# Optimization experiments

Hardware: AMD Instinct MI355X
Metric: run time of the kernel (lower is better)

Reference implementation:

```python
import jax, jax.numpy as jnp
import numpy as np

TEMPERATURE = 0.05
BETA = 1.0
LAMBDA_THRESHOLD = 0.7


def setup_inputs() -> dict:
    key = jax.random.key(0)
    k1, k2 = jax.random.split(key)
    B, D = 8192, 256
    features = jax.random.normal(k1, (B, D), dtype=jnp.float32)
    labels = jax.random.randint(k2, (B,), 0, 100, dtype=jnp.int64)
    return {"features": features, "labels": labels}


def reference(features, labels):
    B = features.shape[0]
    eps = 1e-12
    # L2 normalize rows
    f = features / jnp.maximum(jnp.linalg.norm(features, axis=1, keepdims=True), eps)
    sim = jnp.matmul(f, f.T) / TEMPERATURE                      # [B, B]
    sim_max = jnp.max(sim, axis=1, keepdims=True)               # [B, 1]
    sim_stable = sim - sim_max

    same = (labels[:, None] == labels[None, :])
    eye = jnp.eye(B, dtype=bool)
    pos_mask = same & ~eye                                       # [B, B] bool

    # Denominator: logsumexp over all non-self entries per row
    exp_sim = jnp.exp(sim_stable) * (~eye)
    log_denom = jnp.log(jnp.sum(exp_sim, axis=1, keepdims=True) + eps) + sim_max  # [B,1]

    # SCL term: mean over positive pairs of (log_denom[i] - sim[i,j])
    pos_f = pos_mask.astype(sim.dtype)
    n_pos = jnp.sum(pos_f)
    scl_sum = jnp.sum(pos_f * (log_denom - sim))
    scl_loss = jnp.where(n_pos > 0, scl_sum / jnp.maximum(n_pos, 1.0), 0.0)

    # Relaxation term: per row, logsumexp over high-sim positive logits + baseline
    high = (sim * TEMPERATURE > LAMBDA_THRESHOLD) & pos_mask     # [B, B] bool
    neg_inf = jnp.asarray(-jnp.inf, sim.dtype)
    masked_logits = jnp.where(high, sim_stable, neg_inf)          # [B, B]
    baseline = (1.0 / TEMPERATURE) - sim_max                      # [B, 1]
    all_logits = jnp.concatenate([masked_logits, baseline], axis=1)  # [B, B+1]
    row_lse = jax.nn.logsumexp(all_logits, axis=1)                # [B]
    row_has = jnp.any(high, axis=1)
    n_high = jnp.sum(high.astype(sim.dtype))
    relax_sum = jnp.sum(jnp.where(row_has, row_lse, 0.0))
    relaxation_loss = jnp.where(n_high > 0, relax_sum / jnp.maximum(n_high, 1.0), 0.0)

    total = scl_loss + BETA * relaxation_loss
    return jnp.clip(total, 0.0, 10.0)
```

## Files before the change

### kernel.cpp

```cpp
#include <hip/hip_runtime.h>
#include <hip/hip_bf16.h>
#include <math.h>

#define B_N 8192
#define D_K 256
#define TILE 128
#define NT 512
#define NBLK 64
#define NPAIR 2080
#define NCLS 100
#define KEXP 28.8539008177792681f
#define KCH 32
#define NCHUNK 8

typedef __attribute__((ext_vector_type(8))) short short8;
typedef __attribute__((ext_vector_type(4))) float f32x4;

template <bool V> struct BoolC { static constexpr bool value = V; };

__device__ __forceinline__ unsigned short f2bf(float x) {
    unsigned int u = __float_as_uint(x);
    unsigned int r = (u + 0x7FFFu + ((u >> 16) & 1u)) >> 16;
    return (unsigned short)r;
}

__device__ __forceinline__ void gload_lds16(const short* g, short* l) {
    __builtin_amdgcn_global_load_lds(
        (const __attribute__((address_space(1))) void*)g,
        (__attribute__((address_space(3))) void*)l, 16, 0, 0);
}

__device__ __forceinline__ float row_sum16(float v) {
    v += __int_as_float(__builtin_amdgcn_update_dpp(0, __float_as_int(v), 0xB1, 0xF, 0xF, true));
    v += __int_as_float(__builtin_amdgcn_update_dpp(0, __float_as_int(v), 0x4E, 0xF, 0xF, true));
    v += __int_as_float(__builtin_amdgcn_update_dpp(0, __float_as_int(v), 0x141, 0xF, 0xF, true));
    v += __int_as_float(__builtin_amdgcn_update_dpp(0, __float_as_int(v), 0x140, 0xF, 0xF, true));
    return v;
}

__global__ void prep_kernel(const float* __restrict__ feat, unsigned short* __restrict__ fnorm,
                            const int* __restrict__ labels, int* __restrict__ cnt,
                            float* __restrict__ gscal, double* __restrict__ accum,
                            unsigned int* __restrict__ done) {
    if (blockIdx.x == 0) {
        __shared__ int h[NCLS];
        int t = threadIdx.x;
        if (t < NCLS) h[t] = 0;
        if (t == 0) {
            gscal[0] = 0.f; gscal[1] = 0.f;
            accum[0] = 0.0; accum[1] = 0.0; accum[2] = 0.0;
            *done = 0u;
        }
        __syncthreads();
        for (int r = t; r < B_N; r += 256) atomicAdd(&h[labels[r]], 1);
        __syncthreads();
        if (t < NCLS) cnt[t] = h[t];
    }
    int wave = threadIdx.x >> 6, lane = threadIdx.x & 63;
    int row = blockIdx.x * 4 + wave;
    float4 v = *(const float4*)(feat + (size_t)row * D_K + lane * 4);
    float ss = v.x * v.x + v.y * v.y + v.z * v.z + v.w * v.w;
    #pragma unroll
    for (int off = 1; off < 64; off <<= 1) ss += __shfl_xor(ss, off);
    float inv = 1.0f / fmaxf(sqrtf(ss), 1e-12f);
    ushort4 o;
    o.x = f2bf(v.x * inv); o.y = f2bf(v.y * inv);
    o.z = f2bf(v.z * inv); o.w = f2bf(v.w * inv);
    *(ushort4*)(fnorm + (size_t)row * D_K + lane * 4) = o;
}

#define WAITV(N) asm volatile("s_waitcnt vmcnt(" #N ")" ::: "memory")
#define BARX() __builtin_amdgcn_s_barrier()

__global__ __launch_bounds__(NT, 4) void main_kernel(
        const unsigned short* __restrict__ fnorm, const int* __restrict__ labels,
        float2* __restrict__ G, float* __restrict__ gscal) {
    int bid = blockIdx.x;
    int b = (int)((sqrtf(8.0f * bid + 1.0f) - 1.0f) * 0.5f);
    while ((b + 1) * (b + 2) / 2 <= bid) ++b;
    while (b * (b + 1) / 2 > bid) --b;
    int a = bid - b * (b + 1) / 2;
    const int row0 = a * TILE, col0 = b * TILE;
    const bool diag = (a == b);

    __shared__ short As[4][TILE * KCH];
    __shared__ short Bs[4][TILE * KCH];
    __shared__ int Ls[2 * TILE];
    __shared__ float2 Rbuf[4 * TILE];
    __shared__ float2 Cbuf[2 * TILE];
    __shared__ int ghs[8];
    __shared__ float gps[8];

    const int tid = threadIdx.x;
    const int lane = tid & 63, wave = tid >> 6;
    const int wm = wave >> 2, wn = wave & 3;
    const int l15 = lane & 15, lhi = lane >> 4;
    const short* fn = (const short*)fnorm;

    const int rs = tid >> 2, cs = (tid & 3) ^ ((tid >> 3) & 3);
    const int uds = (tid & ~63) * 8;
    const int abase = (row0 + rs) * D_K + cs * 8;
    const int bbase = (col0 + rs) * D_K + cs * 8;

    if (tid < 128) Ls[tid] = labels[row0 + tid];
    else if (tid < 256) Ls[tid] = labels[col0 + tid - 128];
    if (lane == 0) ghs[wave] = 0;

    const int ch8 = (lhi ^ ((l15 >> 1) & 3)) * 8;
    int aoff[4], boff[2];
    #pragma unroll
    for (int mi = 0; mi < 4; mi++) aoff[mi] = (wm * 64 + mi * 16 + l15) * KCH + ch8;
    #pragma unroll
    for (int ni = 0; ni < 2; ni++) boff[ni] = (wn * 32 + ni * 16 + l15) * KCH + ch8;

    f32x4 acc[4][2];
    #pragma unroll
    for (int i = 0; i < 4; i++)
        #pragma unroll
        for (int j = 0; j < 2; j++) acc[i][j] = {0.f, 0.f, 0.f, 0.f};

#define ISSUE_AB(kc2) { gload_lds16(fn + abase + (kc2) * KCH, &As[(kc2) & 3][uds]); \
                        gload_lds16(fn + bbase + (kc2) * KCH, &Bs[(kc2) & 3][uds]); }
#define ISSUE_A(kc2)  { gload_lds16(fn + abase + (kc2) * KCH, &As[(kc2) & 3][uds]); }
#define COMPUTE(kc, BSRC) { \
    const short* Ap = As[(kc) & 3]; \
    const short* Bp = BSRC[(kc) & 3]; \
    short8 af[4], bfr[2]; \
    _Pragma("unroll") for (int mi = 0; mi < 4; mi++) af[mi] = *(const short8*)&Ap[aoff[mi]]; \
    _Pragma("unroll") for (int ni = 0; ni < 2; ni++) bfr[ni] = *(const short8*)&Bp[boff[ni]]; \
    __builtin_amdgcn_s_setprio(1); \
    _Pragma("unroll") for (int mi = 0; mi < 4; mi++) \
        _Pragma("unroll") for (int ni = 0; ni < 2; ni++) \
            acc[mi][ni] = __builtin_amdgcn_mfma_f32_16x16x32_bf16(af[mi], bfr[ni], acc[mi][ni], 0, 0, 0); \
    __builtin_amdgcn_s_setprio(0); }

    if (!diag) {
        ISSUE_AB(0) ISSUE_AB(1)
        ISSUE_AB(2) WAITV(4); BARX(); COMPUTE(0, Bs)
        ISSUE_AB(3) WAITV(4); BARX(); COMPUTE(1, Bs)
        ISSUE_AB(4) WAITV(4); BARX(); COMPUTE(2, Bs)
        ISSUE_AB(5) WAITV(4); BARX(); COMPUTE(3, Bs)
        ISSUE_AB(6) WAITV(4); BARX(); COMPUTE(4, Bs)
        ISSUE_AB(7) WAITV(4); BARX(); COMPUTE(5, Bs)
                    WAITV(2); BARX(); COMPUTE(6, Bs)
                    WAITV(0); BARX(); COMPUTE(7, Bs)
    } else {
        ISSUE_A(0) ISSUE_A(1)
        ISSUE_A(2) WAITV(2); BARX(); COMPUTE(0, As)
        ISSUE_A(3) WAITV(2); BARX(); COMPUTE(1, As)
        ISSUE_A(4) WAITV(2); BARX(); COMPUTE(2, As)
        ISSUE_A(5) WAITV(2); BARX(); COMPUTE(3, As)
        ISSUE_A(6) WAITV(2); BARX(); COMPUTE(4, As)
        ISSUE_A(7) WAITV(2); BARX(); COMPUTE(5, As)
                   WAITV(1); BARX(); COMPUTE(6, As)
                   WAITV(0); BARX(); COMPUTE(7, As)
    }

    int lc[2], colg[2];
    #pragma unroll
    for (int ni = 0; ni < 2; ni++) {
        int c = wn * 32 + ni * 16 + l15;
        lc[ni] = Ls[128 + c];
        colg[ni] = col0 + c;
    }

    auto body = [&](auto DIAGC) {
        constexpr bool DIAG = decltype(DIAGC)::value;
        float cD[2] = {0.f, 0.f};
        float gp = 0.f;
        bool anyhi = false;

        #pragma unroll
        for (int mi = 0; mi < 4; mi++) {
            #pragma unroll
            for (int reg = 0; reg < 4; reg++) {
                int rloc = wm * 64 + mi * 16 + lhi * 4 + reg;
                int rowg = row0 + rloc;
                int lr = Ls[rloc];
                float d = 0.f;
                #pragma unroll
                for (int ni = 0; ni < 2; ni++) {
                    float dot = acc[mi][ni][reg];
                    float e = __builtin_exp2f((dot - 1.0f) * KEXP);
                    bool ns = !DIAG || (rowg != colg[ni]);
                    float ev = ns ? e : 0.f;
                    d += ev; cD[ni] += ev;
                    bool ps = ns && (lr == lc[ni]);
                    gp += ps ? dot : 0.f;
                    anyhi = anyhi | (ps & (dot > 0.7f));
                }
                d = row_sum16(d);
                if (l15 == 0) Rbuf[wn * 128 + rloc] = {d, 0.f};
            }
        }

        if (!DIAG) {
            #pragma unroll
            for (int ni = 0; ni < 2; ni++) {
                cD[ni] += __shfl_xor(cD[ni], 16);
                cD[ni] += __shfl_xor(cD[ni], 32);
            }
            if (lhi == 0) {
                #pragma unroll
                for (int ni = 0; ni < 2; ni++)
                    Cbuf[wm * 128 + wn * 32 + ni * 16 + l15] = {cD[ni], 0.f};
            }
        }

        gp = row_sum16(gp);
        gp += __shfl_xor(gp, 16);
        gp += __shfl_xor(gp, 32);
        if (lane == 0) gps[wave] = gp;

        if (__any(anyhi)) {
            float cR[2] = {0.f, 0.f};
            int nhi = 0;
            #pragma unroll
            for (int mi = 0; mi < 4; mi++) {
                #pragma unroll
                for (int reg = 0; reg < 4; reg++) {
                    int rloc = wm * 64 + mi * 16 + lhi * 4 + reg;
                    int rowg = row0 + rloc;
                    int lr = Ls[rloc];
                    float rx = 0.f;
                    #pragma unroll
                    for (int ni = 0; ni < 2; ni++) {
                        float dot = acc[mi][ni][reg];
                        bool ns = !DIAG || (rowg != colg[ni]);
                        bool hi = ns && (lr == lc[ni]) && (dot > 0.7f);
                        float e = hi ? __builtin_exp2f((dot - 1.0f) * KEXP) : 0.f;
                        rx += e; cR[ni] += e; nhi += hi ? 1 : 0;
                    }
                    rx = row_sum16(rx);
                    if (l15 == 0) Rbuf[wn * 128 + rloc].y = rx;
                }
            }
            if (!DIAG) {
                #pragma unroll
                for (int ni = 0; ni < 2; ni++) {
                    cR[ni] += __shfl_xor(cR[ni], 16);
                    cR[ni] += __shfl_xor(cR[ni], 32);
                }
                if (lhi == 0) {
                    #pragma unroll
                    for (int ni = 0; ni < 2; ni++)
                        Cbuf[wm * 128 + wn * 32 + ni * 16 + l15].y = cR[ni];
                }
            }
            #pragma unroll
            for (int off = 1; off < 64; off <<= 1) nhi += __shfl_xor(nhi, off);
            if (lane == 0) ghs[wave] = nhi;
        }
    };
    if (diag) body(BoolC<true>{});
    else body(BoolC<false>{});
    __syncthreads();

    if (tid < 128) {
        int r = tid;
        float2 a0 = Rbuf[r], a1 = Rbuf[128 + r], a2 = Rbuf[256 + r], a3 = Rbuf[384 + r];
        G[(size_t)b * B_N + row0 + r] = {a0.x + a1.x + a2.x + a3.x, a0.y + a1.y + a2.y + a3.y};
    } else if (tid < 256 && !diag) {
        int c = tid - 128;
        float2 a0 = Cbuf[c], a1 = Cbuf[128 + c];
        G[(size_t)a * B_N + col0 + c] = {a0.x + a1.x, a0.y + a1.y};
    }
    if (tid == 0) {
        float w = diag ? 1.0f : 2.0f;
        float gpt = gps[0] + gps[1] + gps[2] + gps[3] + gps[4] + gps[5] + gps[6] + gps[7];
        atomicAdd(&gscal[0], w * gpt);
        int tot = ghs[0] + ghs[1] + ghs[2] + ghs[3] + ghs[4] + ghs[5] + ghs[6] + ghs[7];
        if (tot > 0) atomicAdd(&gscal[1], w * (float)tot);
    }
}

__global__ void finalize_kernel(const float2* __restrict__ G, const int* __restrict__ labels,
                                const int* __restrict__ cnt, const float* __restrict__ gscal,
                                double* __restrict__ accum, unsigned int* __restrict__ done,
                                float* __restrict__ out) {
    int lane = threadIdx.x & 63, q = threadIdx.x >> 6;
    int r = blockIdx.x * 64 + lane;
    float d = 0.f, rx = 0.f;
    #pragma unroll
    for (int s = 0; s < 16; ++s) {
        float2 g = G[(size_t)(q * 16 + s) * B_N + r];
        d += g.x; rx += g.y;
    }
    __shared__ float2 sh[4][64];
    sh[q][lane] = {d, rx};
    __syncthreads();
    if (threadIdx.x < 64) {
        int rr = blockIdx.x * 64 + threadIdx.x;
        float2 t0 = sh[0][threadIdx.x], t1 = sh[1][threadIdx.x];
        float2 t2 = sh[2][threadIdx.x], t3 = sh[3][threadIdx.x];
        float dd = t0.x + t1.x + t2.x + t3.x;
        float rr2 = t0.y + t1.y + t2.y + t3.y;
        float np = (float)(cnt[labels[rr]] - 1);
        float ld = logf(dd + 1e-12f) + 20.0f;
        double s1 = (double)np * (double)ld;
        double s2 = (double)np;
        double s3 = (rr2 > 0.f) ? (double)logf(rr2 + 1.0f) : 0.0;
        #pragma unroll
        for (int off = 1; off < 64; off <<= 1) {
            s1 += __shfl_xor(s1, off);
            s2 += __shfl_xor(s2, off);
            s3 += __shfl_xor(s3, off);
        }
        if (threadIdx.x == 0) {
            atomicAdd(&accum[0], s1);
            atomicAdd(&accum[1], s2);
            atomicAdd(&accum[2], s3);
            __threadfence();
            unsigned int tk = atomicAdd(done, 1u);
            if (tk == gridDim.x - 1) {
                double a1 = atomicAdd(&accum[0], 0.0);
                double a2 = atomicAdd(&accum[1], 0.0);
                double a3 = atomicAdd(&accum[2], 0.0);
                double gp = (double)gscal[0];
                double gh = (double)gscal[1];
                double scl = (a2 > 0.0) ? (a1 - 20.0 * gp) / fmax(a2, 1.0) : 0.0;
                double rel = (gh > 0.0) ? a3 / fmax(gh, 1.0) : 0.0;
                double tot = scl + rel;
                tot = fmin(fmax(tot, 0.0), 10.0);
                out[0] = (float)tot;
            }
        }
    }
}

extern "C" void kernel_launch(void* const* d_in, const int* in_sizes, int n_in,
                              void* d_out, int out_size, void* d_ws, size_t ws_size,
                              hipStream_t stream) {
    const float* feat = (const float*)d_in[0];
    const int* labels = (const int*)d_in[1];
    float* out = (float*)d_out;
    char* ws = (char*)d_ws;

    unsigned short* fnorm = (unsigned short*)(ws);
    float2* G          = (float2*)(ws + (size_t)4 * 1024 * 1024);
    int*    cnt        = (int*)(ws + (size_t)8 * 1024 * 1024);
    float*  gscal      = (float*)(ws + (size_t)8 * 1024 * 1024 + 1024);
    double* accum      = (double*)(ws + (size_t)8 * 1024 * 1024 + 2048);
    unsigned int* done = (unsigned int*)(ws + (size_t)8 * 1024 * 1024 + 3072);

    prep_kernel<<<B_N / 4, 256, 0, stream>>>(feat, fnorm, labels, cnt, gscal, accum, done);
    main_kernel<<<NPAIR, NT, 0, stream>>>(fnorm, labels, G, gscal);
    finalize_kernel<<<B_N / 64, 256, 0, stream>>>(G, labels, cnt, gscal, accum, done, out);
    (void)in_sizes; (void)n_in; (void)out_size; (void)ws_size;
}
```

Before: 121.6 us.

## Make main kernel persistent and prefetch next tile's loads during epilogue

Launches a fixed grid of 512 blocks that loop over the triangular tile pairs instead of one block per pair. During the last K-chunks of the current tile it issues the global-to-LDS loads for the next tile, so the exp/reduction epilogue overlaps with memory latency. Diagonal tiles now load B separately instead of reusing A, adding a little extra traffic. The static round-robin assignment may leave some blocks with one more tile than others.

```diff
diff --git a/kernel.cpp b/kernel.cpp
--- a/kernel.cpp
+++ b/kernel.cpp
@@ -12,6 +12,7 @@
 #define KEXP 28.8539008177792681f
 #define KCH 32
 #define NCHUNK 8
+#define GRID_MAIN 512
 
 typedef __attribute__((ext_vector_type(8))) short short8;
 typedef __attribute__((ext_vector_type(4))) float f32x4;
@@ -36,6 +37,14 @@
     v += __int_as_float(__builtin_amdgcn_update_dpp(0, __float_as_int(v), 0x141, 0xF, 0xF, true));
     v += __int_as_float(__builtin_amdgcn_update_dpp(0, __float_as_int(v), 0x140, 0xF, 0xF, true));
     return v;
+}
+
+__device__ __forceinline__ void decode_pair(int t, int& a, int& b) {
+    int bb = (int)((sqrtf(8.0f * t + 1.0f) - 1.0f) * 0.5f);
+    while ((bb + 1) * (bb + 2) / 2 <= t) ++bb;
+    while (bb * (bb + 1) / 2 > t) --bb;
+    a = t - bb * (bb + 1) / 2;
+    b = bb;
 }
 
 __global__ void prep_kernel(const float* __restrict__ feat, unsigned short* __restrict__ fnorm,
@@ -71,18 +80,11 @@
 
 #define WAITV(N) asm volatile("s_waitcnt vmcnt(" #N ")" ::: "memory")
 #define BARX() __builtin_amdgcn_s_barrier()
+#define LGKB() { asm volatile("s_waitcnt lgkmcnt(0)" ::: "memory"); __builtin_amdgcn_s_barrier(); }
 
 __global__ __launch_bounds__(NT, 4) void main_kernel(
         const unsigned short* __restrict__ fnorm, const int* __restrict__ labels,
         float2* __restrict__ G, float* __restrict__ gscal) {
-    int bid = blockIdx.x;
-    int b = (int)((sqrtf(8.0f * bid + 1.0f) - 1.0f) * 0.5f);
-    while ((b + 1) * (b + 2) / 2 <= bid) ++b;
-    while (b * (b + 1) / 2 > bid) --b;
-    int a = bid - b * (b + 1) / 2;
-    const int row0 = a * TILE, col0 = b * TILE;
-    const bool diag = (a == b);
-
     __shared__ short As[4][TILE * KCH];
     __shared__ short Bs[4][TILE * KCH];
     __shared__ int Ls[2 * TILE];
@@ -99,12 +101,7 @@
 
     const int rs = tid >> 2, cs = (tid & 3) ^ ((tid >> 3) & 3);
     const int uds = (tid & ~63) * 8;
-    const int abase = (row0 + rs) * D_K + cs * 8;
-    const int bbase = (col0 + rs) * D_K + cs * 8;
-
-    if (tid < 128) Ls[tid] = labels[row0 + tid];
-    else if (tid < 256) Ls[tid] = labels[col0 + tid - 128];
-    if (lane == 0) ghs[wave] = 0;
+    const int stg = rs * D_K + cs * 8;
 
     const int ch8 = (lhi ^ ((l15 >> 1) & 3)) * 8;
     int aoff[4], boff[2];
@@ -113,18 +110,24 @@
     #pragma unroll
     for (int ni = 0; ni < 2; ni++) boff[ni] = (wn * 32 + ni * 16 + l15) * KCH + ch8;
 
-    f32x4 acc[4][2];
-    #pragma unroll
-    for (int i = 0; i < 4; i++)
-        #pragma unroll
-        for (int j = 0; j < 2; j++) acc[i][j] = {0.f, 0.f, 0.f, 0.f};
-
-#define ISSUE_AB(kc2) { gload_lds16(fn + abase + (kc2) * KCH, &As[(kc2) & 3][uds]); \
-                        gload_lds16(fn + bbase + (kc2) * KCH, &Bs[(kc2) & 3][uds]); }
-#define ISSUE_A(kc2)  { gload_lds16(fn + abase + (kc2) * KCH, &As[(kc2) & 3][uds]); }
-#define COMPUTE(kc, BSRC) { \
+    int t = blockIdx.x, a, b;
+    decode_pair(t, a, b);
+    int row0 = a * TILE, col0 = b * TILE;
+    bool diag = (a == b);
+    int abase = row0 * D_K + stg;
+    int bbase = col0 * D_K + stg;
+
+    if (tid < 128) Ls[tid] = labels[row0 + tid];
+    else if (tid < 256) Ls[tid] = labels[col0 + tid - 128];
+    if (lane == 0) ghs[wave] = 0;
+
+#define ISSUE(kc)  { gload_lds16(fn + abase + (kc) * KCH, &As[(kc) & 3][uds]); \
+                     gload_lds16(fn + bbase + (kc) * KCH, &Bs[(kc) & 3][uds]); }
+#define ISSUE_N(c) { gload_lds16(fn + nabase + (c) * KCH, &As[(c) & 3][uds]); \
+                     gload_lds16(fn + nbbase + (c) * KCH, &Bs[(c) & 3][uds]); }
+#define COMPUTE(kc) { \
     const short* Ap = As[(kc) & 3]; \
-    const short* Bp = BSRC[(kc) & 3]; \
+    const short* Bp = Bs[(kc) & 3]; \
     short8 af[4], bfr[2]; \
     _Pragma("unroll") for (int mi = 0; mi < 4; mi++) af[mi] = *(const short8*)&Ap[aoff[mi]]; \
     _Pragma("unroll") for (int ni = 0; ni < 2; ni++) bfr[ni] = *(const short8*)&Bp[boff[ni]]; \
@@ -134,87 +137,43 @@
             acc[mi][ni] = __builtin_amdgcn_mfma_f32_16x16x32_bf16(af[mi], bfr[ni], acc[mi][ni], 0, 0, 0); \
     __builtin_amdgcn_s_setprio(0); }
 
-    if (!diag) {
-        ISSUE_AB(0) ISSUE_AB(1)
-        ISSUE_AB(2) WAITV(4); BARX(); COMPUTE(0, Bs)
-        ISSUE_AB(3) WAITV(4); BARX(); COMPUTE(1, Bs)
-        ISSUE_AB(4) WAITV(4); BARX(); COMPUTE(2, Bs)
-        ISSUE_AB(5) WAITV(4); BARX(); COMPUTE(3, Bs)
-        ISSUE_AB(6) WAITV(4); BARX(); COMPUTE(4, Bs)
-        ISSUE_AB(7) WAITV(4); BARX(); COMPUTE(5, Bs)
-                    WAITV(2); BARX(); COMPUTE(6, Bs)
-                    WAITV(0); BARX(); COMPUTE(7, Bs)
-    } else {
-        ISSUE_A(0) ISSUE_A(1)
-        ISSUE_A(2) WAITV(2); BARX(); COMPUTE(0, As)
-        ISSUE_A(3) WAITV(2); BARX(); COMPUTE(1, As)
-        ISSUE_A(4) WAITV(2); BARX(); COMPUTE(2, As)
-        ISSUE_A(5) WAITV(2); BARX(); COMPUTE(3, As)
-        ISSUE_A(6) WAITV(2); BARX(); COMPUTE(4, As)
-        ISSUE_A(7) WAITV(2); BARX(); COMPUTE(5, As)
-                   WAITV(1); BARX(); COMPUTE(6, As)
-                   WAITV(0); BARX(); COMPUTE(7, As)
-    }
-
-    int lc[2], colg[2];
-    #pragma unroll
-    for (int ni = 0; ni < 2; ni++) {
-        int c = wn * 32 + ni * 16 + l15;
-        lc[ni] = Ls[128 + c];
-        colg[ni] = col0 + c;
-    }
-
-    auto body = [&](auto DIAGC) {
-        constexpr bool DIAG = decltype(DIAGC)::value;
-        float cD[2] = {0.f, 0.f};
-        float gp = 0.f;
-        bool anyhi = false;
-
+    ISSUE(0) ISSUE(1) ISSUE(2)
+
+    for (;;) {
+        f32x4 acc[4][2];
         #pragma unroll
-        for (int mi = 0; mi < 4; mi++) {
+        for (int i = 0; i < 4; i++)
             #pragma unroll
-            for (int reg = 0; reg < 4; reg++) {
-                int rloc = wm * 64 + mi * 16 + lhi * 4 + reg;
-                int rowg = row0 + rloc;
-                int lr = Ls[rloc];
-                float d = 0.f;
-                #pragma unroll
-                for (int ni = 0; ni < 2; ni++) {
-                    float dot = acc[mi][ni][reg];
-                    float e = __builtin_exp2f((dot - 1.0f) * KEXP);
-                    bool ns = !DIAG || (rowg != colg[ni]);
-                    float ev = ns ? e : 0.f;
-                    d += ev; cD[ni] += ev;
-                    bool ps = ns && (lr == lc[ni]);
-                    gp += ps ? dot : 0.f;
-                    anyhi = anyhi | (ps & (dot > 0.7f));
-                }
-                d = row_sum16(d);
-                if (l15 == 0) Rbuf[wn * 128 + rloc] = {d, 0.f};
-            }
-        }
-
-        if (!DIAG) {
-            #pragma unroll
-            for (int ni = 0; ni < 2; ni++) {
-                cD[ni] += __shfl_xor(cD[ni], 16);
-                cD[ni] += __shfl_xor(cD[ni], 32);
-            }
-            if (lhi == 0) {
-                #pragma unroll
-                for (int ni = 0; ni < 2; ni++)
-                    Cbuf[wm * 128 + wn * 32 + ni * 16 + l15] = {cD[ni], 0.f};
-            }
-        }
-
-        gp = row_sum16(gp);
-        gp += __shfl_xor(gp, 16);
-        gp += __shfl_xor(gp, 32);
-        if (lane == 0) gps[wave] = gp;
-
-        if (__any(anyhi)) {
-            float cR[2] = {0.f, 0.f};
-            int nhi = 0;
+            for (int j = 0; j < 2; j++) acc[i][j] = {0.f, 0.f, 0.f, 0.f};
+
+        WAITV(4); BARX(); COMPUTE(0) ISSUE(3)
+        WAITV(4); BARX(); COMPUTE(1) ISSUE(4)
+        WAITV(4); BARX(); COMPUTE(2) ISSUE(5)
+        WAITV(4); BARX(); COMPUTE(3) ISSUE(6)
+        WAITV(4); BARX(); COMPUTE(4) ISSUE(7)
+        const int nt = t + GRID_MAIN;
+        int na, nb2;
+        decode_pair(nt < NPAIR ? nt : 0, na, nb2);
+        const int nrow0 = na * TILE, ncol0 = nb2 * TILE;
+        const int nabase = nrow0 * D_K + stg, nbbase = ncol0 * D_K + stg;
+        WAITV(4); BARX(); COMPUTE(5) ISSUE_N(0)
+        WAITV(4); BARX(); COMPUTE(6) ISSUE_N(1)
+        WAITV(4); BARX(); COMPUTE(7) ISSUE_N(2)
+
+        int lc[2], colg[2];
+        #pragma unroll
+        for (int ni = 0; ni < 2; ni++) {
+            int c = wn * 32 + ni * 16 + l15;
+            lc[ni] = Ls[128 + c];
+            colg[ni] = col0 + c;
+        }
+
+        auto body = [&](auto DIAGC) {
+            constexpr bool DIAG = decltype(DIAGC)::value;
+            float cD[2] = {0.f, 0.f};
+            float gp = 0.f;
+            bool anyhi = false;
+
             #pragma unroll
             for (int mi = 0; mi < 4; mi++) {
                 #pragma unroll
@@ -222,56 +181,113 @@
                     int rloc = wm * 64 + mi * 16 + lhi * 4 + reg;
                     int rowg = row0 + rloc;
                     int lr = Ls[rloc];
-                    float rx = 0.f;
+                    float d = 0.f;
                     #pragma unroll
                     for (int ni = 0; ni < 2; ni++) {
                         float dot = acc[mi][ni][reg];
+                        float e = __builtin_exp2f((dot - 1.0f) * KEXP);
                         bool ns = !DIAG || (rowg != colg[ni]);
-                        bool hi = ns && (lr == lc[ni]) && (dot > 0.7f);
-                        float e = hi ? __builtin_exp2f((dot - 1.0f) * KEXP) : 0.f;
-                        rx += e; cR[ni] += e; nhi += hi ? 1 : 0;
+                        float ev = ns ? e : 0.f;
+                        d += ev; cD[ni] += ev;
+                        bool ps = ns && (lr == lc[ni]);
+                        gp += ps ? dot : 0.f;
+                        anyhi = anyhi | (ps & (dot > 0.7f));
                     }
-                    rx = row_sum16(rx);
-                    if (l15 == 0) Rbuf[wn * 128 + rloc].y = rx;
+                    d = row_sum16(d);
+                    if (l15 == 0) Rbuf[wn * 128 + rloc] = {d, 0.f};
                 }
             }
+
             if (!DIAG) {
                 #pragma unroll
                 for (int ni = 0; ni < 2; ni++) {
-                    cR[ni] += __shfl_xor(cR[ni], 16);
-                    cR[ni] += __shfl_xor(cR[ni], 32);
+                    cD[ni] += __shfl_xor(cD[ni], 16);
+                    cD[ni] += __shfl_xor(cD[ni], 32);
                 }
                 if (lhi == 0) {
                     #pragma unroll
                     for (int ni = 0; ni < 2; ni++)
-                        Cbuf[wm * 128 + wn * 32 + ni * 16 + l15].y = cR[ni];
+                        Cbuf[wm * 128 + wn * 32 + ni * 16 + l15] = {cD[ni], 0.f};
                 }
             }
-            #pragma unroll
-            for (int off = 1; off < 64; off <<= 1) nhi += __shfl_xor(nhi, off);
-            if (lane == 0) ghs[wave] = nhi;
-        }
-    };
-    if (diag) body(BoolC<true>{});
-    else body(BoolC<false>{});
-    __syncthreads();
-
-    if (tid < 128) {
-        int r = tid;
-        float2 a0 = Rbuf[r], a1 = Rbuf[128 + r], a2 = Rbuf[256 + r], a3 = Rbuf[384 + r];
-        G[(size_t)b * B_N + row0 + r] = {a0.x + a1.x + a2.x + a3.x, a0.y + a1.y + a2.y + a3.y};
-    } else if (tid < 256 && !diag) {
-        int c = tid - 128;
-        float2 a0 = Cbuf[c], a1 = Cbuf[128 + c];
-        G[(size_t)a * B_N + col0 + c] = {a0.x + a1.x, a0.y + a1.y};
+
+            gp = row_sum16(gp);
+            gp += __shfl_xor(gp, 16);
+            gp += __shfl_xor(gp, 32);
+            if (lane == 0) gps[wave] = gp;
+
+            if (__any(anyhi)) {
+                float cR[2] = {0.f, 0.f};
+                int nhi = 0;
+                #pragma unroll
+                for (int mi = 0; mi < 4; mi++) {
+                    #pragma unroll
+                    for (int reg = 0; reg < 4; reg++) {
+                        int rloc = wm * 64 + mi * 16 + lhi * 4 + reg;
+                        int rowg = row0 + rloc;
+                        int lr = Ls[rloc];
+                        float rx = 0.f;
+                        #pragma unroll
+                        for (int ni = 0; ni < 2; ni++) {
+                            float dot = acc[mi][ni][reg];
+                            bool ns = !DIAG || (rowg != colg[ni]);
+                            bool hi = ns && (lr == lc[ni]) && (dot > 0.7f);
+                            float e = hi ? __builtin_exp2f((dot - 1.0f) * KEXP) : 0.f;
+                            rx += e; cR[ni] += e; nhi += hi ? 1 : 0;
+                        }
+                        rx = row_sum16(rx);
+                        if (l15 == 0) Rbuf[wn * 128 + rloc].y = rx;
+                    }
+                }
+                if (!DIAG) {
+                    #pragma unroll
+                    for (int ni = 0; ni < 2; ni++) {
+                        cR[ni] += __shfl_xor(cR[ni], 16);
+                        cR[ni] += __shfl_xor(cR[ni], 32);
+                    }
+                    if (lhi == 0) {
+                        #pragma unroll
+                        for (int ni = 0; ni < 2; ni++)
+                            Cbuf[wm * 128 + wn * 32 + ni * 16 + l15].y = cR[ni];
+                    }
+                }
+                #pragma unroll
+                for (int off = 1; off < 64; off <<= 1) nhi += __shfl_xor(nhi, off);
+                if (lane == 0) ghs[wave] = nhi;
+            }
+        };
+        if (diag) body(BoolC<true>{});
+        else body(BoolC<false>{});
+
+        LGKB();
+
+        if (tid < 128) {
+            int r = tid;
+            float2 a0 = Rbuf[r], a1 = Rbuf[128 + r], a2 = Rbuf[256 + r], a3 = Rbuf[384 + r];
+            G[(size_t)b * B_N + row0 + r] = {a0.x + a1.x + a2.x + a3.x, a0.y + a1.y + a2.y + a3.y};
+        } else if (tid < 256 && !diag) {
+            int c = tid - 128;
+            float2 a0 = Cbuf[c], a1 = Cbuf[128 + c];
+            G[(size_t)a * B_N + col0 + c] = {a0.x + a1.x, a0.y + a1.y};
+        }
+        if (tid == 0) {
+            float w = diag ? 1.0f : 2.0f;
+            float gpt = gps[0] + gps[1] + gps[2] + gps[3] + gps[4] + gps[5] + gps[6] + gps[7];
+            atomicAdd(&gscal[0], w * gpt);
+            int tot = ghs[0] + ghs[1] + ghs[2] + ghs[3] + ghs[4] + ghs[5] + ghs[6] + ghs[7];
+            if (tot > 0) atomicAdd(&gscal[1], w * (float)tot);
+        }
+
+        LGKB();
+
+        if (nt >= NPAIR) break;
+        t = nt; a = na; b = nb2; row0 = nrow0; col0 = ncol0; diag = (na == nb2);
+        abase = nabase; bbase = nbbase;
+        if (tid < 128) Ls[tid] = labels[row0 + tid];
+        else if (tid < 256) Ls[tid] = labels[col0 + tid - 128];
+        if (lane == 0) ghs[wave] = 0;
     }
-    if (tid == 0) {
-        float w = diag ? 1.0f : 2.0f;
-        float gpt = gps[0] + gps[1] + gps[2] + gps[3] + gps[4] + gps[5] + gps[6] + gps[7];
-        atomicAdd(&gscal[0], w * gpt);
-        int tot = ghs[0] + ghs[1] + ghs[2] + ghs[3] + ghs[4] + ghs[5] + ghs[6] + ghs[7];
-        if (tot > 0) atomicAdd(&gscal[1], w * (float)tot);
-    }
+    WAITV(0);
 }
 
 __global__ void finalize_kernel(const float2* __restrict__ G, const int* __restrict__ labels,
@@ -344,7 +360,7 @@
     unsigned int* done = (unsigned int*)(ws + (size_t)8 * 1024 * 1024 + 3072);
 
     prep_kernel<<<B_N / 4, 256, 0, stream>>>(feat, fnorm, labels, cnt, gscal, accum, done);
-    main_kernel<<<NPAIR, NT, 0, stream>>>(fnorm, labels, G, gscal);
+    main_kernel<<<GRID_MAIN, NT, 0, stream>>>(fnorm, labels, G, gscal);
     finalize_kernel<<<B_N / 64, 256, 0, stream>>>(G, labels, cnt, gscal, accum, done, out);
     (void)in_sizes; (void)n_in; (void)out_size; (void)ws_size;
 }
```

Measured after the change: 121.9 us. No clear change (+0.2%).
